# Kernel tuning notes

Hardware: AMD Instinct MI355X
Metric: run time of the kernel (lower is better)

The kernel has to match this reference:

```python
import jax, jax.numpy as jnp
import numpy as np
from jax import lax

B, T, D, H = 4096, 256, 18, 32


def setup_inputs() -> dict:
    key = jax.random.key(0)
    ks = jax.random.split(key, 9)
    s = 1.0 / np.sqrt(H)  # PyTorch LSTM init scale
    return {
        "batch": jax.random.normal(ks[0], (B, T, D), dtype=jnp.float32),
        "W_ih": jax.random.normal(ks[1], (4 * H, D), dtype=jnp.float32) * s,
        "W_hh": jax.random.normal(ks[2], (4 * H, H), dtype=jnp.float32) * s,
        "b_ih": jax.random.normal(ks[3], (4 * H,), dtype=jnp.float32) * s,
        "b_hh": jax.random.normal(ks[4], (4 * H,), dtype=jnp.float32) * s,
        "W1": jax.random.normal(ks[5], (512, H * T), dtype=jnp.float32) * 0.02,
        "b1": jax.random.normal(ks[6], (512,), dtype=jnp.float32) * 0.02,
        "W2": jax.random.normal(ks[7], (1, 512), dtype=jnp.float32) * 0.02,
        "b2": jax.random.normal(ks[8], (1,), dtype=jnp.float32) * 0.02,
    }


def _lstm(batch, W_ih, W_hh, b_ih, b_hh):
    b, t, _ = batch.shape
    h = batch.dtype.type
    # Precompute input projections for all timesteps: [B, T, 4H]
    x_proj = jnp.einsum('bti,gi->btg', batch, W_ih) + b_ih + b_hh
    W_hh_T = W_hh.T  # [H, 4H]

    def step(carry, xp):
        h_prev, c_prev = carry
        gates = xp + h_prev @ W_hh_T  # [B, 4H]
        i, f, g, o = jnp.split(gates, 4, axis=-1)  # PyTorch gate order i,f,g,o
        i = jax.nn.sigmoid(i)
        f = jax.nn.sigmoid(f)
        g = jnp.tanh(g)
        o = jax.nn.sigmoid(o)
        c = f * c_prev + i * g
        h_new = o * jnp.tanh(c)
        return (h_new, c), h_new

    h0 = jnp.zeros((b, H), dtype=batch.dtype)
    c0 = jnp.zeros((b, H), dtype=batch.dtype)
    _, hs = lax.scan(step, (h0, c0), x_proj.transpose(1, 0, 2))  # hs: [T, B, H]
    return hs.transpose(1, 0, 2)  # [B, T, H]


def reference(batch, W_ih, W_hh, b_ih, b_hh, W1, b1, W2, b2):
    hs = _lstm(batch, W_ih, W_hh, b_ih, b_hh)            # [B, T, H]
    flat = hs.reshape(hs.shape[0], -1)                   # [B, T*H]
    hid = jax.nn.relu(flat @ W1.T + b1)                  # [B, 512]
    return hid @ W2.T + b2                               # [B, 1]
```

## Files before the change

### kernel.cpp

```cpp
#include <hip/hip_runtime.h>
#include <hip/hip_bf16.h>
#include <stdint.h>

typedef float f32x4 __attribute__((ext_vector_type(4)));
typedef _Float16 half8 __attribute__((ext_vector_type(8)));

#define B_ 4096
#define T_ 256
#define D_ 18
#define H_ 32
#define GK 8192
#define GN 512
#define KSPLIT 4
#define SLOT 520

#define K1_ 1.442695041f
#define K2_ 2.885390082f
#define X2_ __builtin_amdgcn_exp2f
#define RCP_ __builtin_amdgcn_rcpf

__device__ __forceinline__ void ldsbar() {
  asm volatile("s_waitcnt lgkmcnt(0)\n\ts_barrier" ::: "memory");
}
__device__ __forceinline__ void gl_lds16(const _Float16* g, _Float16* l) {
  __builtin_amdgcn_global_load_lds(
      (const __attribute__((address_space(1))) unsigned int*)g,
      (__attribute__((address_space(3))) unsigned int*)l, 16, 0, 0);
}

__global__ __launch_bounds__(256) void cvtw1_kernel(const float* __restrict__ w1,
                                                    unsigned short* __restrict__ dst) {
  int i = blockIdx.x * 256 + threadIdx.x;
  float4 v = ((const float4*)w1)[i];
  unsigned short a = __builtin_bit_cast(unsigned short, (_Float16)v.x);
  unsigned short b = __builtin_bit_cast(unsigned short, (_Float16)v.y);
  unsigned short c = __builtin_bit_cast(unsigned short, (_Float16)v.z);
  unsigned short d = __builtin_bit_cast(unsigned short, (_Float16)v.w);
  uint2 o; o.x = (unsigned)a | ((unsigned)b << 16); o.y = (unsigned)c | ((unsigned)d << 16);
  ((uint2*)dst)[i] = o;
}

__global__ __launch_bounds__(512) void lstm_kernel(
    const float* __restrict__ batch, const float* __restrict__ W_ih,
    const float* __restrict__ W_hh, const float* __restrict__ b_ih,
    const float* __restrict__ b_hh, _Float16* __restrict__ hs) {
  __shared__ _Float16 hist[16 * SLOT];
  __shared__ _Float16 xs[2 * 4096];

  const int tid = (int)threadIdx.x;
  const int lane = tid & 63;
  const int w = tid >> 6;
  const int lq = lane >> 4;
  const int lr = lane & 15;
  const int b0 = (int)blockIdx.x * 16;

  half8 wx, wh;
  {
    int grow = (lr & 3) * 32 + w * 4 + (lr >> 2);
#pragma unroll
    for (int j = 0; j < 8; ++j) {
      int k = lq * 8 + j;
      wx[j] = (k < D_) ? (_Float16)W_ih[grow * D_ + k] : (_Float16)0.0f;
      wh[j] = (_Float16)W_hh[grow * H_ + k];
    }
  }
  f32x4 bias4;
#pragma unroll
  for (int r = 0; r < 4; ++r) {
    int g = r * 32 + w * 4 + lq;
    bias4[r] = b_ih[g] + b_hh[g];
  }

  const int rdo = lr * 32 + ((lq ^ ((lr >> 1) & 3)) << 3);
  const int kcol = w * 4 + lq;
  const int wro = lr * 32 + ((((kcol >> 3) ^ ((lr >> 1) & 3))) << 3) + (kcol & 7);

  const int fe = tid >> 5;
  const int fs = (tid >> 2) & 7;
  const int fg = tid & 3;
  const int fl_rd = fs * SLOT + fe * 32 + ((fg ^ ((fe >> 1) & 3)) << 3);
  _Float16* fl_wp = hs + (size_t)(b0 + fe) * GK + fs * H_ + fg * 8;

  const int e0 = tid / 36, q0 = tid - e0 * 36;
  const int i1 = tid + 512;
  const int e1 = i1 / 36, q1 = i1 - e1 * 36;
  const float* xld0 = batch + (size_t)(b0 + e0) * (T_ * D_) + q0 * 4;
  const float* xld1 = batch + (size_t)(b0 + e1) * (T_ * D_) + q1 * 4;
  float4 xv0, xv1;

#define XLOAD(tb)                                                              \
  do {                                                                         \
    xv0 = *(const float4*)(xld0 + (tb) * 144);                                 \
    if (tid < 64) xv1 = *(const float4*)(xld1 + (tb) * 144);                   \
  } while (0)

#define XPUT(E, Q, V, buf)                                                     \
  do {                                                                         \
    int swz_ = ((E) >> 1) & 3;                                                 \
    _Pragma("unroll") for (int j = 0; j < 4; ++j) {                            \
      int f_ = (Q) * 4 + j;                                                    \
      int to_ = (f_ * 57) >> 10;                          \
      int d_ = f_ - to_ * 18;                                                  \
      float val_ = (j == 0) ? (V).x : (j == 1) ? (V).y : (j == 2) ? (V).z : (V).w; \
      xs[(buf) * 4096 + to_ * 512 + (E) * 32 + (((d_ >> 3) ^ swz_) << 3) + (d_ & 7)] = \
          (_Float16)val_;                                                      \
    }                                                                          \
  } while (0)

#define XSTORE(buf)                                                            \
  do {                                                                         \
    XPUT(e0, q0, xv0, buf);                                                    \
    if (tid < 64) XPUT(e1, q1, xv1, buf);                                      \
  } while (0)

#define STEP(tt, AXC, PRE)                                                     \
  do {                                                                         \
    _Float16* hrd = ((tt) == 0 ? po + 7 * SLOT : pr + ((tt)-1) * SLOT);        \
    half8 hf = *(const half8*)&hrd[rdo];                                       \
    f32x4 acc = __builtin_amdgcn_mfma_f32_16x16x32_f16(wh, hf, AXC, 0, 0, 0);  \
    PRE;                                                                       \
    float ei = X2_(-K1_ * acc[0]);                                             \
    float ef = X2_(-K1_ * acc[1]);                                             \
    float eg = X2_(-K2_ * acc[2]);                                             \
    float eo = X2_(-K1_ * acc[3]);                                             \
    float pi_ = (1.0f + ei) * (1.0f + eg);                                     \
    float num = fmaf(c, pi_, (1.0f + ef) * (1.0f - eg));                       \
    c = num * RCP_((1.0f + ef) * pi_);                                         \
    float ec = X2_(-K2_ * c);                                                  \
    float h = (1.0f - ec) * RCP_((1.0f + eo) * (1.0f + ec));                   \
    pr[(tt)*SLOT + wro] = (_Float16)h;                                         \
    ldsbar();                                                                  \
  } while (0)

  XLOAD(0);
  for (int i = tid; i < 16 * SLOT; i += 512) hist[i] = (_Float16)0.0f;
  for (int i = tid; i < 8192; i += 512) xs[i] = (_Float16)0.0f;
  ldsbar();
  XSTORE(0);
  XLOAD(1);
  ldsbar();

  float c = 0.0f;
  for (int blk = 0; blk < 32; ++blk) {
    const int p = blk & 1;
    _Float16* pr = hist + p * (8 * SLOT);
    _Float16* po = hist + (p ^ 1) * (8 * SLOT);
    const int xo = p * 4096;

    half8 xq[8];
#pragma unroll
    for (int j = 0; j < 8; ++j) xq[j] = *(const half8*)&xs[xo + j * 512 + rdo];
    f32x4 ax0, ax1;
    ax0 = __builtin_amdgcn_mfma_f32_16x16x32_f16(wx, xq[0], bias4, 0, 0, 0);

    STEP(0, ax0, ax1 = __builtin_amdgcn_mfma_f32_16x16x32_f16(wx, xq[1], bias4, 0, 0, 0));
    STEP(1, ax1, ax0 = __builtin_amdgcn_mfma_f32_16x16x32_f16(wx, xq[2], bias4, 0, 0, 0));
    STEP(2, ax0, ax1 = __builtin_amdgcn_mfma_f32_16x16x32_f16(wx, xq[3], bias4, 0, 0, 0));
    STEP(3, ax1, ax0 = __builtin_amdgcn_mfma_f32_16x16x32_f16(wx, xq[4], bias4, 0, 0, 0));
    if (blk < 31) XSTORE(p ^ 1);
    if (blk < 30) XLOAD(blk + 2);
    STEP(4, ax0, ax1 = __builtin_amdgcn_mfma_f32_16x16x32_f16(wx, xq[5], bias4, 0, 0, 0));
    if (blk) {
      half8 hv = *(const half8*)&hist[(p ^ 1) * (8 * SLOT) + fl_rd];
      *(half8*)(fl_wp + (size_t)(blk - 1) * (8 * H_)) = hv;
    }
    STEP(5, ax1, ax0 = __builtin_amdgcn_mfma_f32_16x16x32_f16(wx, xq[6], bias4, 0, 0, 0));
    STEP(6, ax0, ax1 = __builtin_amdgcn_mfma_f32_16x16x32_f16(wx, xq[7], bias4, 0, 0, 0));
    STEP(7, ax1, );
  }
  {
    half8 hv = *(const half8*)&hist[8 * SLOT + fl_rd];
    *(half8*)(fl_wp + (size_t)31 * (8 * H_)) = hv;
  }
#undef STEP
#undef XSTORE
#undef XPUT
#undef XLOAD
}

__global__ __launch_bounds__(256, 2) void gemm_kernel(
    const _Float16* __restrict__ Ahs, const _Float16* __restrict__ Bw1,
    float* __restrict__ part) {
  __shared__ _Float16 As[2 * 128 * 64];
  __shared__ _Float16 Bs[2 * 128 * 64];

  const int bid = (int)blockIdx.x;
  const int m0 = (bid & 31) << 7;
  const int n0 = ((bid >> 5) & 3) << 7;
  const int ksp = bid >> 7;
  const int k0 = ksp << 11;
  float* outp = part + (size_t)ksp * ((size_t)B_ * GN);

  const int tid = (int)threadIdx.x;
  const int lane = tid & 63, w = tid >> 6;
  const int wm = w & 1, wn = w >> 1;
  const int lq = lane >> 4, lr = lane & 15;

  const _Float16* gA[4]; const _Float16* gB[4];
  _Float16* lA[4]; _Float16* lB[4];
#pragma unroll
  for (int j = 0; j < 4; ++j) {
    int p = tid + 256 * j;
    int row = p >> 3, q = p & 7, cg = q ^ (row & 7);
    gA[j] = Ahs + (size_t)(m0 + row) * GK + k0 + cg * 8;
    gB[j] = Bw1 + (size_t)(n0 + row) * GK + k0 + cg * 8;
    int wbase = (w * 64 + 256 * j) * 8;
    lA[j] = As + wbase;
    lB[j] = Bs + wbase;
  }

  int offA[4][2], offB[4][2];
#pragma unroll
  for (int mt = 0; mt < 4; ++mt)
#pragma unroll
    for (int ks = 0; ks < 2; ++ks) {
      int m = wm * 64 + mt * 16 + lr;
      offA[mt][ks] = m * 64 + (((lq + ks * 4) ^ (m & 7)) << 3);
      int n = wn * 64 + mt * 16 + lr;
      offB[mt][ks] = n * 64 + (((lq + ks * 4) ^ (n & 7)) << 3);
    }

  f32x4 acc[4][4];
#pragma unroll
  for (int mt = 0; mt < 4; ++mt)
#pragma unroll
    for (int nt = 0; nt < 4; ++nt) {
      acc[mt][nt][0] = 0.f; acc[mt][nt][1] = 0.f;
      acc[mt][nt][2] = 0.f; acc[mt][nt][3] = 0.f;
    }

#define STAGE(POFF)                                                            \
  do {                                                                         \
    _Pragma("unroll") for (int j = 0; j < 4; ++j) {                            \
      gl_lds16(gA[j], lA[j] + (POFF));                                         \
      gl_lds16(gB[j], lB[j] + (POFF));                                         \
      gA[j] += 64; gB[j] += 64;                                                \
    }                                                                          \
  } while (0)

#define FRAGS(POFF)                                                            \
  half8 af[4][2], bf[4][2];                                                    \
  _Pragma("unroll") for (int mt = 0; mt < 4; ++mt)                             \
    _Pragma("unroll") for (int ks = 0; ks < 2; ++ks) {                         \
      af[mt][ks] = *(const half8*)&As[(POFF) + offA[mt][ks]];                  \
      bf[mt][ks] = *(const half8*)&Bs[(POFF) + offB[mt][ks]];                  \
    }

#define MFMAS                                                                  \
  _Pragma("unroll") for (int ks = 0; ks < 2; ++ks)                             \
    _Pragma("unroll") for (int mt = 0; mt < 4; ++mt)                           \
      _Pragma("unroll") for (int nt = 0; nt < 4; ++nt)                         \
        acc[mt][nt] = __builtin_amdgcn_mfma_f32_16x16x32_f16(                  \
            af[mt][ks], bf[nt][ks], acc[mt][nt], 0, 0, 0);

  STAGE(0);
  STAGE(8192);

  for (int it = 0; it < 31; ++it) {
    const int POFF = (it & 1) * 8192;
    asm volatile("s_waitcnt vmcnt(8)\n\ts_barrier" ::: "memory");
    FRAGS(POFF);
    asm volatile("s_waitcnt lgkmcnt(0)\n\ts_barrier" ::: "memory");
    if (it < 30) STAGE(POFF);
    MFMAS;
  }
  {
    asm volatile("s_waitcnt vmcnt(0)\n\ts_barrier" ::: "memory");
    FRAGS(8192);
    MFMAS;
  }
#undef MFMAS
#undef FRAGS
#undef STAGE

#pragma unroll
  for (int mt = 0; mt < 4; ++mt)
#pragma unroll
    for (int nt = 0; nt < 4; ++nt) {
      int n = n0 + wn * 64 + nt * 16 + lr;
#pragma unroll
      for (int r = 0; r < 4; ++r) {
        int m = m0 + wm * 64 + mt * 16 + lq * 4 + r;
        outp[(size_t)m * GN + n] = acc[mt][nt][r];
      }
    }
}

__global__ __launch_bounds__(256) void head_kernel(const float* __restrict__ part,
                                                   const float* __restrict__ b1,
                                                   const float* __restrict__ W2,
                                                   const float* __restrict__ b2,
                                                   float* __restrict__ out) {
  const int b = (int)(blockIdx.x * 4 + (threadIdx.x >> 6));
  const int l = (int)(threadIdx.x & 63);
  const size_t stride = (size_t)B_ * GN;
  const float4* b14 = (const float4*)b1;
  const float4* w4 = (const float4*)W2;
  float s = 0.0f;
#pragma unroll
  for (int p = 0; p < 2; ++p) {
    int i = p * 64 + l;
    float4 hv = ((const float4*)(part + (size_t)b * GN))[i];
#pragma unroll
    for (int sp = 1; sp < KSPLIT; ++sp) {
      float4 pv = ((const float4*)(part + sp * stride + (size_t)b * GN))[i];
      hv.x += pv.x; hv.y += pv.y; hv.z += pv.z; hv.w += pv.w;
    }
    float4 bv = b14[i], wv = w4[i];
    float t0 = fmaxf(hv.x + bv.x, 0.0f);
    float t1 = fmaxf(hv.y + bv.y, 0.0f);
    float t2 = fmaxf(hv.z + bv.z, 0.0f);
    float t3 = fmaxf(hv.w + bv.w, 0.0f);
    s = fmaf(t0, wv.x, s); s = fmaf(t1, wv.y, s);
    s = fmaf(t2, wv.z, s); s = fmaf(t3, wv.w, s);
  }
#pragma unroll
  for (int off = 32; off >= 1; off >>= 1) s += __shfl_xor(s, off);
  if (l == 0) out[b] = s + b2[0];
}

extern "C" void kernel_launch(void* const* d_in, const int* in_sizes, int n_in,
                              void* d_out, int out_size, void* d_ws, size_t ws_size,
                              hipStream_t stream) {
  const float* batch = (const float*)d_in[0];
  const float* W_ih = (const float*)d_in[1];
  const float* W_hh = (const float*)d_in[2];
  const float* b_ih = (const float*)d_in[3];
  const float* b_hh = (const float*)d_in[4];
  const float* W1 = (const float*)d_in[5];
  const float* b1 = (const float*)d_in[6];
  const float* W2 = (const float*)d_in[7];
  const float* b2 = (const float*)d_in[8];
  float* out = (float*)d_out;

  char* ws = (char*)d_ws;
  _Float16* hs = (_Float16*)ws;
  _Float16* w1h = (_Float16*)(ws + 67108864);
  float* part = (float*)(ws + 67108864 + 8388608);

  cvtw1_kernel<<<4096, 256, 0, stream>>>(W1, (unsigned short*)w1h);
  lstm_kernel<<<256, 512, 0, stream>>>(batch, W_ih, W_hh, b_ih, b_hh, hs);
  gemm_kernel<<<512, 256, 0, stream>>>(hs, w1h, part);
  head_kernel<<<1024, 256, 0, stream>>>(part, b1, W2, b2, out);
}
```

Measured before the change: 224.5 us.

## Make each LSTM wave own four batch rows to remove block barriers

The LSTM kernel is restructured so each wave independently processes 4 batch elements, holding all 8 gate tiles of W_hh/W_ih in registers, instead of 8 waves splitting the gate dimension for 16 elements and syncing with s_barrier every timestep. This removes the per-timestep workgroup barrier and cross-wave LDS exchange, relying on intra-wave ordering through per-wave LDS. In exchange each wave issues 16 MFMAs per step and the input projection MFMAs are recomputed inline. Only 4 of every 16 lanes do the activation math, and block size drops to 256 threads with much higher register pressure.

```diff
diff --git a/kernel.cpp b/kernel.cpp
--- a/kernel.cpp
+++ b/kernel.cpp
@@ -12,16 +12,12 @@
 #define GK 8192
 #define GN 512
 #define KSPLIT 4
-#define SLOT 520
 
 #define K1_ 1.442695041f
 #define K2_ 2.885390082f
 #define X2_ __builtin_amdgcn_exp2f
 #define RCP_ __builtin_amdgcn_rcpf
 
-__device__ __forceinline__ void ldsbar() {
-  asm volatile("s_waitcnt lgkmcnt(0)\n\ts_barrier" ::: "memory");
-}
 __device__ __forceinline__ void gl_lds16(const _Float16* g, _Float16* l) {
   __builtin_amdgcn_global_load_lds(
       (const __attribute__((address_space(1))) unsigned int*)g,
@@ -40,139 +36,151 @@
   ((uint2*)dst)[i] = o;
 }
 
-__global__ __launch_bounds__(512) void lstm_kernel(
+__global__ __launch_bounds__(256, 1) void lstm_kernel(
     const float* __restrict__ batch, const float* __restrict__ W_ih,
     const float* __restrict__ W_hh, const float* __restrict__ b_ih,
     const float* __restrict__ b_hh, _Float16* __restrict__ hs) {
-  __shared__ _Float16 hist[16 * SLOT];
-  __shared__ _Float16 xs[2 * 4096];
+  __shared__ _Float16 hist[4][2048];
+  __shared__ _Float16 xs[4][2048];
 
   const int tid = (int)threadIdx.x;
   const int lane = tid & 63;
   const int w = tid >> 6;
   const int lq = lane >> 4;
   const int lr = lane & 15;
-  const int b0 = (int)blockIdx.x * 16;
-
-  half8 wx, wh;
-  {
-    int grow = (lr & 3) * 32 + w * 4 + (lr >> 2);
+  const int er = lr & 3;
+  const int swz = (lr >> 1) & 3;
+  const int be = (int)blockIdx.x * 16 + w * 4;
+  _Float16* hw = &hist[w][0];
+  _Float16* xw = &xs[w][0];
+
+  half8 wh[8], wx[8];
+  f32x4 bias[8];
+#pragma unroll
+  for (int mt = 0; mt < 8; ++mt) {
+    int G = (lr & 3) * 32 + mt * 4 + (lr >> 2);
 #pragma unroll
     for (int j = 0; j < 8; ++j) {
       int k = lq * 8 + j;
-      wx[j] = (k < D_) ? (_Float16)W_ih[grow * D_ + k] : (_Float16)0.0f;
-      wh[j] = (_Float16)W_hh[grow * H_ + k];
-    }
-  }
-  f32x4 bias4;
-#pragma unroll
-  for (int r = 0; r < 4; ++r) {
-    int g = r * 32 + w * 4 + lq;
-    bias4[r] = b_ih[g] + b_hh[g];
-  }
-
-  const int rdo = lr * 32 + ((lq ^ ((lr >> 1) & 3)) << 3);
-  const int kcol = w * 4 + lq;
-  const int wro = lr * 32 + ((((kcol >> 3) ^ ((lr >> 1) & 3))) << 3) + (kcol & 7);
-
-  const int fe = tid >> 5;
-  const int fs = (tid >> 2) & 7;
-  const int fg = tid & 3;
-  const int fl_rd = fs * SLOT + fe * 32 + ((fg ^ ((fe >> 1) & 3)) << 3);
-  _Float16* fl_wp = hs + (size_t)(b0 + fe) * GK + fs * H_ + fg * 8;
-
-  const int e0 = tid / 36, q0 = tid - e0 * 36;
-  const int i1 = tid + 512;
-  const int e1 = i1 / 36, q1 = i1 - e1 * 36;
-  const float* xld0 = batch + (size_t)(b0 + e0) * (T_ * D_) + q0 * 4;
-  const float* xld1 = batch + (size_t)(b0 + e1) * (T_ * D_) + q1 * 4;
-  float4 xv0, xv1;
+      wh[mt][j] = (_Float16)W_hh[G * H_ + k];
+      wx[mt][j] = (k < D_) ? (_Float16)W_ih[G * D_ + k] : (_Float16)0.0f;
+    }
+#pragma unroll
+    for (int r = 0; r < 4; ++r) {
+      int g = r * 32 + mt * 4 + lq;
+      bias[mt][r] = b_ih[g] + b_hh[g];
+    }
+  }
+
+  const int rdo = er * 32 + ((lq ^ swz) << 3);
+
+  const int f1i = lane + 64, f2i = lane + 128;
+  const int e0 = lane / 36, q0 = lane - e0 * 36;
+  const int e1 = f1i / 36, q1 = f1i - e1 * 36;
+  const int e2 = f2i / 36, q2 = f2i - e2 * 36;
+  const float* xld0 = batch + (size_t)(be + e0) * (T_ * D_) + q0 * 4;
+  const float* xld1 = batch + (size_t)(be + e1) * (T_ * D_) + q1 * 4;
+  const float* xld2 = batch + (size_t)(be + e2) * (T_ * D_) + q2 * 4;
+  float4 xv0, xv1, xv2;
 
 #define XLOAD(tb)                                                              \
   do {                                                                         \
     xv0 = *(const float4*)(xld0 + (tb) * 144);                                 \
-    if (tid < 64) xv1 = *(const float4*)(xld1 + (tb) * 144);                   \
+    xv1 = *(const float4*)(xld1 + (tb) * 144);                                 \
+    if (lane < 16) xv2 = *(const float4*)(xld2 + (tb) * 144);                  \
   } while (0)
 
 #define XPUT(E, Q, V, buf)                                                     \
   do {                                                                         \
-    int swz_ = ((E) >> 1) & 3;                                                 \
     _Pragma("unroll") for (int j = 0; j < 4; ++j) {                            \
       int f_ = (Q) * 4 + j;                                                    \
-      int to_ = (f_ * 57) >> 10;                          \
-      int d_ = f_ - to_ * 18;                                                  \
+      int t_ = (f_ * 57) >> 10;                           \
+      int d_ = f_ - t_ * 18;                                                   \
       float val_ = (j == 0) ? (V).x : (j == 1) ? (V).y : (j == 2) ? (V).z : (V).w; \
-      xs[(buf) * 4096 + to_ * 512 + (E) * 32 + (((d_ >> 3) ^ swz_) << 3) + (d_ & 7)] = \
-          (_Float16)val_;                                                      \
+      xw[(buf) * 1024 + t_ * 128 + (E) * 32 + (((d_ >> 3) ^ ((E) >> 1)) << 3) + \
+         (d_ & 7)] = (_Float16)val_;                                           \
     }                                                                          \
   } while (0)
 
 #define XSTORE(buf)                                                            \
   do {                                                                         \
     XPUT(e0, q0, xv0, buf);                                                    \
-    if (tid < 64) XPUT(e1, q1, xv1, buf);                                      \
+    XPUT(e1, q1, xv1, buf);                                                    \
+    if (lane < 16) XPUT(e2, q2, xv2, buf);                                     \
   } while (0)
 
-#define STEP(tt, AXC, PRE)                                                     \
-  do {                                                                         \
-    _Float16* hrd = ((tt) == 0 ? po + 7 * SLOT : pr + ((tt)-1) * SLOT);        \
-    half8 hf = *(const half8*)&hrd[rdo];                                       \
-    f32x4 acc = __builtin_amdgcn_mfma_f32_16x16x32_f16(wh, hf, AXC, 0, 0, 0);  \
-    PRE;                                                                       \
-    float ei = X2_(-K1_ * acc[0]);                                             \
-    float ef = X2_(-K1_ * acc[1]);                                             \
-    float eg = X2_(-K2_ * acc[2]);                                             \
-    float eo = X2_(-K1_ * acc[3]);                                             \
-    float pi_ = (1.0f + ei) * (1.0f + eg);                                     \
-    float num = fmaf(c, pi_, (1.0f + ef) * (1.0f - eg));                       \
-    c = num * RCP_((1.0f + ef) * pi_);                                         \
-    float ec = X2_(-K2_ * c);                                                  \
-    float h = (1.0f - ec) * RCP_((1.0f + eo) * (1.0f + ec));                   \
-    pr[(tt)*SLOT + wro] = (_Float16)h;                                         \
-    ldsbar();                                                                  \
-  } while (0)
+  int fl_off[2];
+  _Float16* fl_gp[2];
+#pragma unroll
+  for (int u = 0; u < 2; ++u) {
+    int idx = lane + u * 64;
+    int fe = idx >> 5, ts = (idx >> 2) & 7, cg = idx & 3;
+    fl_off[u] = ts * 128 + fe * 32 + ((cg ^ (fe >> 1)) << 3);
+    fl_gp[u] = hs + (size_t)(be + fe) * GK + ts * 32 + cg * 8;
+  }
 
   XLOAD(0);
-  for (int i = tid; i < 16 * SLOT; i += 512) hist[i] = (_Float16)0.0f;
-  for (int i = tid; i < 8192; i += 512) xs[i] = (_Float16)0.0f;
-  ldsbar();
+  for (int i = lane; i < 1024; i += 64) {
+    ((unsigned*)hw)[i] = 0u;
+    ((unsigned*)xw)[i] = 0u;
+  }
   XSTORE(0);
   XLOAD(1);
-  ldsbar();
-
-  float c = 0.0f;
+
+  float c[8];
+#pragma unroll
+  for (int mt = 0; mt < 8; ++mt) c[mt] = 0.0f;
+
   for (int blk = 0; blk < 32; ++blk) {
     const int p = blk & 1;
-    _Float16* pr = hist + p * (8 * SLOT);
-    _Float16* po = hist + (p ^ 1) * (8 * SLOT);
-    const int xo = p * 4096;
-
     half8 xq[8];
 #pragma unroll
-    for (int j = 0; j < 8; ++j) xq[j] = *(const half8*)&xs[xo + j * 512 + rdo];
-    f32x4 ax0, ax1;
-    ax0 = __builtin_amdgcn_mfma_f32_16x16x32_f16(wx, xq[0], bias4, 0, 0, 0);
-
-    STEP(0, ax0, ax1 = __builtin_amdgcn_mfma_f32_16x16x32_f16(wx, xq[1], bias4, 0, 0, 0));
-    STEP(1, ax1, ax0 = __builtin_amdgcn_mfma_f32_16x16x32_f16(wx, xq[2], bias4, 0, 0, 0));
-    STEP(2, ax0, ax1 = __builtin_amdgcn_mfma_f32_16x16x32_f16(wx, xq[3], bias4, 0, 0, 0));
-    STEP(3, ax1, ax0 = __builtin_amdgcn_mfma_f32_16x16x32_f16(wx, xq[4], bias4, 0, 0, 0));
+    for (int t = 0; t < 8; ++t) xq[t] = *(const half8*)&xw[p * 1024 + t * 128 + rdo];
+
+#pragma unroll
+    for (int tt = 0; tt < 8; ++tt) {
+      const int sw = p * 8 + tt;
+      const int sr = tt ? (sw - 1) : ((p ^ 1) * 8 + 7);
+      half8 hf = *(const half8*)&hw[sr * 128 + rdo];
+      f32x4 acc[8];
+#pragma unroll
+      for (int mt = 0; mt < 8; ++mt) {
+        f32x4 ax = __builtin_amdgcn_mfma_f32_16x16x32_f16(wx[mt], xq[tt], bias[mt], 0, 0, 0);
+        acc[mt] = __builtin_amdgcn_mfma_f32_16x16x32_f16(wh[mt], hf, ax, 0, 0, 0);
+      }
+      if (lr < 4) {
+#pragma unroll
+        for (int mt = 0; mt < 8; ++mt) {
+          float ei = X2_(-K1_ * acc[mt][0]);
+          float ef = X2_(-K1_ * acc[mt][1]);
+          float eg = X2_(-K2_ * acc[mt][2]);
+          float eo = X2_(-K1_ * acc[mt][3]);
+          float pi_ = (1.0f + ei) * (1.0f + eg);
+          float num = fmaf(c[mt], pi_, (1.0f + ef) * (1.0f - eg));
+          c[mt] = num * RCP_((1.0f + ef) * pi_);
+          float ec = X2_(-K2_ * c[mt]);
+          float h = (1.0f - ec) * RCP_((1.0f + eo) * (1.0f + ec));
+          hw[sw * 128 + lr * 32 + (((mt >> 1) ^ (lr >> 1)) << 3) + (mt & 1) * 4 + lq] =
+              (_Float16)h;
+        }
+      }
+    }
     if (blk < 31) XSTORE(p ^ 1);
     if (blk < 30) XLOAD(blk + 2);
-    STEP(4, ax0, ax1 = __builtin_amdgcn_mfma_f32_16x16x32_f16(wx, xq[5], bias4, 0, 0, 0));
     if (blk) {
-      half8 hv = *(const half8*)&hist[(p ^ 1) * (8 * SLOT) + fl_rd];
-      *(half8*)(fl_wp + (size_t)(blk - 1) * (8 * H_)) = hv;
-    }
-    STEP(5, ax1, ax0 = __builtin_amdgcn_mfma_f32_16x16x32_f16(wx, xq[6], bias4, 0, 0, 0));
-    STEP(6, ax0, ax1 = __builtin_amdgcn_mfma_f32_16x16x32_f16(wx, xq[7], bias4, 0, 0, 0));
-    STEP(7, ax1, );
-  }
-  {
-    half8 hv = *(const half8*)&hist[8 * SLOT + fl_rd];
-    *(half8*)(fl_wp + (size_t)31 * (8 * H_)) = hv;
-  }
-#undef STEP
+      const int pp = (blk - 1) & 1;
+#pragma unroll
+      for (int u = 0; u < 2; ++u) {
+        half8 hv = *(const half8*)&hw[pp * 1024 + fl_off[u]];
+        *(half8*)(fl_gp[u] + (size_t)(blk - 1) * 256) = hv;
+      }
+    }
+  }
+#pragma unroll
+  for (int u = 0; u < 2; ++u) {
+    half8 hv = *(const half8*)&hw[1024 + fl_off[u]];
+    *(half8*)(fl_gp[u] + (size_t)31 * 256) = hv;
+  }
 #undef XSTORE
 #undef XPUT
 #undef XLOAD
@@ -339,7 +347,7 @@
   float* part = (float*)(ws + 67108864 + 8388608);
 
   cvtw1_kernel<<<4096, 256, 0, stream>>>(W1, (unsigned short*)w1h);
-  lstm_kernel<<<256, 512, 0, stream>>>(batch, W_ih, W_hh, b_ih, b_hh, hs);
+  lstm_kernel<<<256, 256, 0, stream>>>(batch, W_ih, W_hh, b_ih, b_hh, hs);
   gemm_kernel<<<512, 256, 0, stream>>>(hs, w1h, part);
   head_kernel<<<1024, 256, 0, stream>>>(part, b1, W2, b2, out);
 }
```

After: 346.2 us. 54.2% more time.

## Halve LSTM batch per block, double grid, fuse W1 fp16 conversion into LSTM

Applied to the files above, without the earlier changes.

Each LSTM block now handles 8 batch rows instead of 16, and the grid doubles to 512 blocks so more CUs share the latency-bound recurrence. The MFMA tile still spans 16 columns, so half of every matrix op is padding. The separate W1 fp32-to-fp16 conversion kernel is folded into the LSTM prologue, with each of the 512 blocks converting a 2048-float4 slice, which removes one launch. The risk is that the 16-wide MFMA on 8 rows wastes half its throughput and each block still pays the full serial time-step chain.

```diff
diff --git a/kernel.cpp b/kernel.cpp
--- a/kernel.cpp
+++ b/kernel.cpp
@@ -28,22 +28,11 @@
       (__attribute__((address_space(3))) unsigned int*)l, 16, 0, 0);
 }
 
-__global__ __launch_bounds__(256) void cvtw1_kernel(const float* __restrict__ w1,
-                                                    unsigned short* __restrict__ dst) {
-  int i = blockIdx.x * 256 + threadIdx.x;
-  float4 v = ((const float4*)w1)[i];
-  unsigned short a = __builtin_bit_cast(unsigned short, (_Float16)v.x);
-  unsigned short b = __builtin_bit_cast(unsigned short, (_Float16)v.y);
-  unsigned short c = __builtin_bit_cast(unsigned short, (_Float16)v.z);
-  unsigned short d = __builtin_bit_cast(unsigned short, (_Float16)v.w);
-  uint2 o; o.x = (unsigned)a | ((unsigned)b << 16); o.y = (unsigned)c | ((unsigned)d << 16);
-  ((uint2*)dst)[i] = o;
-}
-
 __global__ __launch_bounds__(512) void lstm_kernel(
     const float* __restrict__ batch, const float* __restrict__ W_ih,
     const float* __restrict__ W_hh, const float* __restrict__ b_ih,
-    const float* __restrict__ b_hh, _Float16* __restrict__ hs) {
+    const float* __restrict__ b_hh, _Float16* __restrict__ hs,
+    const float* __restrict__ w1, unsigned short* __restrict__ w1h) {
   __shared__ _Float16 hist[16 * SLOT];
   __shared__ _Float16 xs[2 * 4096];
 
@@ -52,7 +41,7 @@
   const int w = tid >> 6;
   const int lq = lane >> 4;
   const int lr = lane & 15;
-  const int b0 = (int)blockIdx.x * 16;
+  const int b0 = (int)blockIdx.x * 8;
 
   half8 wx, wh;
   {
@@ -82,16 +71,12 @@
   _Float16* fl_wp = hs + (size_t)(b0 + fe) * GK + fs * H_ + fg * 8;
 
   const int e0 = tid / 36, q0 = tid - e0 * 36;
-  const int i1 = tid + 512;
-  const int e1 = i1 / 36, q1 = i1 - e1 * 36;
   const float* xld0 = batch + (size_t)(b0 + e0) * (T_ * D_) + q0 * 4;
-  const float* xld1 = batch + (size_t)(b0 + e1) * (T_ * D_) + q1 * 4;
-  float4 xv0, xv1;
+  float4 xv0;
 
 #define XLOAD(tb)                                                              \
   do {                                                                         \
-    xv0 = *(const float4*)(xld0 + (tb) * 144);                                 \
-    if (tid < 64) xv1 = *(const float4*)(xld1 + (tb) * 144);                   \
+    if (tid < 288) xv0 = *(const float4*)(xld0 + (tb) * 144);                  \
   } while (0)
 
 #define XPUT(E, Q, V, buf)                                                     \
@@ -109,8 +94,7 @@
 
 #define XSTORE(buf)                                                            \
   do {                                                                         \
-    XPUT(e0, q0, xv0, buf);                                                    \
-    if (tid < 64) XPUT(e1, q1, xv1, buf);                                      \
+    if (tid < 288) XPUT(e0, q0, xv0, buf);                                     \
   } while (0)
 
 #define STEP(tt, AXC, PRE)                                                     \
@@ -138,6 +122,19 @@
   ldsbar();
   XSTORE(0);
   XLOAD(1);
+
+#pragma unroll
+  for (int u = 0; u < 4; ++u) {
+    int i = (int)blockIdx.x * 2048 + u * 512 + tid;
+    float4 v = ((const float4*)w1)[i];
+    unsigned short a = __builtin_bit_cast(unsigned short, (_Float16)v.x);
+    unsigned short b = __builtin_bit_cast(unsigned short, (_Float16)v.y);
+    unsigned short cc = __builtin_bit_cast(unsigned short, (_Float16)v.z);
+    unsigned short d = __builtin_bit_cast(unsigned short, (_Float16)v.w);
+    uint2 o; o.x = (unsigned)a | ((unsigned)b << 16);
+    o.y = (unsigned)cc | ((unsigned)d << 16);
+    ((uint2*)w1h)[i] = o;
+  }
   ldsbar();
 
   float c = 0.0f;
@@ -160,7 +157,7 @@
     if (blk < 31) XSTORE(p ^ 1);
     if (blk < 30) XLOAD(blk + 2);
     STEP(4, ax0, ax1 = __builtin_amdgcn_mfma_f32_16x16x32_f16(wx, xq[5], bias4, 0, 0, 0));
-    if (blk) {
+    if (blk && tid < 256) {
       half8 hv = *(const half8*)&hist[(p ^ 1) * (8 * SLOT) + fl_rd];
       *(half8*)(fl_wp + (size_t)(blk - 1) * (8 * H_)) = hv;
     }
@@ -168,7 +165,7 @@
     STEP(6, ax0, ax1 = __builtin_amdgcn_mfma_f32_16x16x32_f16(wx, xq[7], bias4, 0, 0, 0));
     STEP(7, ax1, );
   }
-  {
+  if (tid < 256) {
     half8 hv = *(const half8*)&hist[8 * SLOT + fl_rd];
     *(half8*)(fl_wp + (size_t)31 * (8 * H_)) = hv;
   }
@@ -338,8 +335,8 @@
   _Float16* w1h = (_Float16*)(ws + 67108864);
   float* part = (float*)(ws + 67108864 + 8388608);
 
-  cvtw1_kernel<<<4096, 256, 0, stream>>>(W1, (unsigned short*)w1h);
-  lstm_kernel<<<256, 512, 0, stream>>>(batch, W_ih, W_hh, b_ih, b_hh, hs);
-  gemm_kernel<<<512, 256, 0, stream>>>(hs, w1h, part);
+  lstm_kernel<<<512, 512, 0, stream>>>(batch, W_ih, W_hh, b_ih, b_hh, hs,
+                                       W1, (unsigned short*)w1h);
+  gemm_kernel<<<512, 256, 0, stream>>>(hs, (const _Float16*)w1h, part);
   head_kernel<<<1024, 256, 0, stream>>>(part, b1, W2, b2, out);
 }
```

Result: slower. 257.6 us (+14.7%).
